# Kernel optimization log

Hardware: AMD Instinct MI355X
Metric: run time of the kernel (lower is better)

## Reference

```python
import jax, jax.numpy as jnp
import numpy as np

B, S, T = 8, 512, 512
E, NHEAD, HD = 512, 8, 64
SRC_VOCAB, TGT_VOCAB, WINDOW = 32000, 8000, 512
LN_EPS = 1e-3  # keras LayerNormalization default


def positional_encoding(length, depth):
    half = depth // 2
    positions = jnp.arange(length, dtype=jnp.float32)[:, None]
    depths = jnp.arange(half, dtype=jnp.float32)[None, :] / (depth / 2)
    angle_rates = 1.0 / (10000.0 ** depths)
    angle_rads = positions * angle_rates  # [length, half]
    return jnp.concatenate([jnp.sin(angle_rads), jnp.cos(angle_rads)], axis=-1)


def layer_norm(x, g, b):
    m = jnp.mean(x, axis=-1, keepdims=True)
    v = jnp.var(x, axis=-1, keepdims=True)
    return (x - m) * jax.lax.rsqrt(v + LN_EPS) * g + b


def mha(xk, xv, xq, wk, wv, wq, dw, db, causal):
    # wk/wv/wq: [H, E, HD] (stacked per-head weights, same math as naive per-head tensordots)
    K = jnp.einsum('bse,hed->bhsd', xk, wk)
    V = jnp.einsum('bse,hed->bhsd', xv, wv)
    Q = jnp.einsum('bqe,hed->bhqd', xq, wq)
    Sk = K.shape[2]
    # NOTE: original divides by sqrt(KEY SEQ LEN), not sqrt(head_dim)
    logits = jnp.einsum('bhqd,bhkd->bhqk', Q, K) / jnp.sqrt(jnp.float32(Sk))
    if causal:
        Sq = Q.shape[2]
        mask = jnp.triu(jnp.full((Sq, Sk), -jnp.inf, dtype=logits.dtype), k=1)
        logits = logits + mask
    w = jax.nn.softmax(logits, axis=-1)
    att = jnp.einsum('bhqk,bhkd->bhqd', w, V)
    b_, h_, q_, d_ = att.shape
    att = att.transpose(0, 2, 1, 3).reshape(b_, q_, h_ * d_)  # concat heads
    return att @ dw + db


def setup_inputs() -> dict:
    key = jax.random.key(0)
    ks = jax.random.split(key, 32)
    n = lambda i, shape, std=0.01: jax.random.normal(ks[i], shape, dtype=jnp.float32) * std
    inp = {
        'src_ids': jax.random.randint(ks[0], (B, S), 0, SRC_VOCAB, dtype=jnp.int32),
        'tgt_ids': jax.random.randint(ks[1], (B, T), 0, TGT_VOCAB, dtype=jnp.int32),
        'src_emb': n(2, (SRC_VOCAB, E), 0.05),
        'tgt_emb': n(3, (TGT_VOCAB, E), 0.05),
        # encoder block
        'enc_wk': n(4, (NHEAD, E, HD)), 'enc_wv': n(5, (NHEAD, E, HD)), 'enc_wq': n(6, (NHEAD, E, HD)),
        'enc_dw': n(7, (E, E), 0.02), 'enc_db': jnp.zeros((E,), jnp.float32),
        'enc_ffw': n(8, (E, E), 0.02), 'enc_ffb': jnp.zeros((E,), jnp.float32),
        'enc_ln_g': jnp.ones((E,), jnp.float32), 'enc_ln_b': jnp.zeros((E,), jnp.float32),
        # decoder block: self-attn, cross-attn, ff, shared ln
        'dec_swk': n(9, (NHEAD, E, HD)), 'dec_swv': n(10, (NHEAD, E, HD)), 'dec_swq': n(11, (NHEAD, E, HD)),
        'dec_sdw': n(12, (E, E), 0.02), 'dec_sdb': jnp.zeros((E,), jnp.float32),
        'dec_cwk': n(13, (NHEAD, E, HD)), 'dec_cwv': n(14, (NHEAD, E, HD)), 'dec_cwq': n(15, (NHEAD, E, HD)),
        'dec_cdw': n(16, (E, E), 0.02), 'dec_cdb': jnp.zeros((E,), jnp.float32),
        'dec_ffw': n(17, (E, E), 0.02), 'dec_ffb': jnp.zeros((E,), jnp.float32),
        'dec_ln_g': jnp.ones((E,), jnp.float32), 'dec_ln_b': jnp.zeros((E,), jnp.float32),
        # classifier
        'cls_w1': n(18, (E, 2 * TGT_VOCAB), 0.02), 'cls_b1': jnp.zeros((2 * TGT_VOCAB,), jnp.float32),
        'cls_w2': n(19, (2 * TGT_VOCAB, TGT_VOCAB), 0.02), 'cls_b2': jnp.zeros((TGT_VOCAB,), jnp.float32),
    }
    return inp


def reference(src_ids, tgt_ids, src_emb, tgt_emb,
              enc_wk, enc_wv, enc_wq, enc_dw, enc_db, enc_ffw, enc_ffb, enc_ln_g, enc_ln_b,
              dec_swk, dec_swv, dec_swq, dec_sdw, dec_sdb,
              dec_cwk, dec_cwv, dec_cwq, dec_cdw, dec_cdb,
              dec_ffw, dec_ffb, dec_ln_g, dec_ln_b,
              cls_w1, cls_b1, cls_w2, cls_b2):
    pos = positional_encoding(WINDOW, E)
    scale = jnp.sqrt(jnp.float32(E))
    x = src_emb[src_ids] * scale + pos[:src_ids.shape[1]]
    y = tgt_emb[tgt_ids] * scale + pos[:tgt_ids.shape[1]]

    # encoder block (self-attn is CAUSALLY masked in original: use_mask=True hardcoded)
    a = mha(x, x, x, enc_wk, enc_wv, enc_wq, enc_dw, enc_db, causal=True)
    h = layer_norm(x + a, enc_ln_g, enc_ln_b)
    f = h @ enc_ffw + enc_ffb
    enc_out = layer_norm(h + f, enc_ln_g, enc_ln_b)

    # decoder block
    sa = mha(y, y, y, dec_swk, dec_swv, dec_swq, dec_sdw, dec_sdb, causal=True)
    h1 = layer_norm(sa + y, dec_ln_g, dec_ln_b)
    ca = mha(enc_out, enc_out, h1, dec_cwk, dec_cwv, dec_cwq, dec_cdw, dec_cdb, causal=False)
    h2 = layer_norm(ca + h1, dec_ln_g, dec_ln_b)
    f2 = h2 @ dec_ffw + dec_ffb
    dec_out = jax.nn.relu(layer_norm(f2 + h2, dec_ln_g, dec_ln_b))

    # classifier
    hid = jax.nn.relu(dec_out @ cls_w1 + cls_b1)
    return hid @ cls_w2 + cls_b2
```

## Files before the change

kernel.cpp:

```cpp
#include <hip/hip_runtime.h>

#define SEQ 512
#define EDIM 512
#define NHEAD 8
#define HDIM 64
#define NBATCH 8
#define ROWS (NBATCH * SEQ)
#define QKV_N (3 * EDIM)
#define TGTV 8000
#define HID2 16000
#define LN_EPS 1e-3f

#define BM 128
#define BN 128
#define BK 32

typedef unsigned short u16;
typedef __bf16 bf16x8 __attribute__((ext_vector_type(8)));
typedef float f32x4 __attribute__((ext_vector_type(4)));

__device__ __forceinline__ float b2f(u16 x) {
  unsigned int u = ((unsigned int)x) << 16;
  float f;
  __builtin_memcpy(&f, &u, 4);
  return f;
}
__device__ __forceinline__ u16 f2b(float f) {
  unsigned int u;
  __builtin_memcpy(&u, &f, 4);
  u = (u + 0x7fffu + ((u >> 16) & 1u)) >> 16;
  return (u16)u;
}

__device__ __forceinline__ void async_copy16(const void* g, void* l) {
  __builtin_amdgcn_global_load_lds(
      (const __attribute__((address_space(1))) unsigned int*)g,
      (__attribute__((address_space(3))) unsigned int*)l, 16, 0, 0);
}

__global__ __launch_bounds__(256) void gemm_bt(
    const u16* __restrict__ A, const u16* __restrict__ B, void* __restrict__ C,
    const float* __restrict__ bias, int M, int N, int K, int lda, int ldb,
    int ldc, long abb, long abh, long bbb, long bbh, long cbb, long cbh,
    int nbh, int flags) {
  __shared__ __align__(16) u16 lsA[BM * BK];
  __shared__ __align__(16) u16 lsB[BN * BK];
  const int tid = threadIdx.x;
  const int wave = tid >> 6, lane = tid & 63;
  const int quad = lane >> 4, l16 = lane & 15;
  const int wm = (wave & 1) << 6, wn = (wave >> 1) << 6;

  const int z = blockIdx.z;
  const int zb = z / nbh, zh = z - zb * nbh;
  const u16* Ab = A + zb * abb + zh * abh;
  const u16* Bb = B + zb * bbb + zh * bbh;
  const long coff = zb * cbb + zh * cbh;
  const int m0 = blockIdx.y * BM, n0 = blockIdx.x * BN;

  f32x4 acc[4][4];
#pragma unroll
  for (int i = 0; i < 4; ++i)
#pragma unroll
    for (int j = 0; j < 4; ++j) acc[i][j] = (f32x4)0.0f;

  const int srow = tid >> 2;
  const int skc = (tid & 3) << 3;
  const u16* ga0 = Ab + (long)(m0 + srow) * lda + skc;
  const u16* ga1 = ga0 + 64L * lda;
  const u16* gb0 = Bb + (long)(n0 + srow) * ldb + skc;
  const u16* gb1 = gb0 + 64L * ldb;
  u16* la0 = &lsA[(wave << 6) * 8];
  u16* la1 = &lsA[(256 + (wave << 6)) * 8];
  u16* lb0 = &lsB[(wave << 6) * 8];
  u16* lb1 = &lsB[(256 + (wave << 6)) * 8];

  for (int k0 = 0; k0 < K; k0 += BK) {
    async_copy16(ga0 + k0, la0);
    async_copy16(ga1 + k0, la1);
    async_copy16(gb0 + k0, lb0);
    async_copy16(gb1 + k0, lb1);
    __syncthreads();
    bf16x8 af[4], bfr[4];
#pragma unroll
    for (int i = 0; i < 4; ++i)
      af[i] = *(const bf16x8*)&lsA[(wm + (i << 4) + l16) * BK + (quad << 3)];
#pragma unroll
    for (int j = 0; j < 4; ++j)
      bfr[j] = *(const bf16x8*)&lsB[(wn + (j << 4) + l16) * BK + (quad << 3)];
#pragma unroll
    for (int i = 0; i < 4; ++i)
#pragma unroll
      for (int j = 0; j < 4; ++j)
        acc[i][j] = __builtin_amdgcn_mfma_f32_16x16x32_bf16(af[i], bfr[j],
                                                            acc[i][j], 0, 0, 0);
    __syncthreads();
  }

  const int relu = flags & 1, obf = flags & 2;
  float bv[4];
#pragma unroll
  for (int j = 0; j < 4; ++j) {
    int col = n0 + wn + (j << 4) + l16;
    bv[j] = (bias != nullptr && col < N) ? bias[col] : 0.0f;
  }
#pragma unroll
  for (int i = 0; i < 4; ++i) {
    int rbase = m0 + wm + (i << 4) + (quad << 2);
#pragma unroll
    for (int j = 0; j < 4; ++j) {
      int col = n0 + wn + (j << 4) + l16;
      if (col < N) {
#pragma unroll
        for (int r = 0; r < 4; ++r) {
          float v = acc[i][j][r] + bv[j];
          if (relu) v = fmaxf(v, 0.0f);
          long idx = coff + (long)(rbase + r) * ldc + col;
          if (obf)
            ((u16*)C)[idx] = f2b(v);
          else
            ((float*)C)[idx] = v;
        }
      }
    }
  }
}

__device__ __forceinline__ float cvt_f(float x) { return x; }
__device__ __forceinline__ float cvt_f(u16 x) { return b2f(x); }

template <typename T>
__global__ __launch_bounds__(256) void transpose_k(
    const T* __restrict__ in, u16* __restrict__ out, int K, int N, int in_ld,
    int out_ld, long ib0, long ib1, long ob0, long ob1, int nb1) {
  __shared__ float tile[32][33];
  const int z = blockIdx.z;
  const int b0 = z / nb1, b1 = z - b0 * nb1;
  const T* ip = in + b0 * ib0 + b1 * ib1;
  u16* op = out + b0 * ob0 + b1 * ob1;
  const int tx = threadIdx.x & 31, ty = threadIdx.x >> 5;
  const int n = blockIdx.x * 32 + tx;
  const int kb = blockIdx.y * 32;
#pragma unroll
  for (int i = ty; i < 32; i += 8) {
    int k = kb + i;
    if (k < K && n < N) tile[i][tx] = cvt_f(ip[(long)k * in_ld + n]);
  }
  __syncthreads();
  const int k2 = kb + tx;
#pragma unroll
  for (int i = ty; i < 32; i += 8) {
    int n2 = blockIdx.x * 32 + i;
    if (k2 < K && n2 < N) op[(long)n2 * out_ld + k2] = f2b(tile[tx][i]);
  }
}

__device__ __forceinline__ float wave_red_max(float v) {
#pragma unroll
  for (int o = 32; o > 0; o >>= 1) v = fmaxf(v, __shfl_xor(v, o, 64));
  return v;
}
__device__ __forceinline__ float wave_red_sum(float v) {
#pragma unroll
  for (int o = 32; o > 0; o >>= 1) v += __shfl_xor(v, o, 64);
  return v;
}

__global__ __launch_bounds__(256) void softmax_k(const float* __restrict__ Sc,
                                                 u16* __restrict__ P,
                                                 int causal) {
  __shared__ float red[4];
  const int row = blockIdx.x;
  const int q = row & (SEQ - 1);
  const float* s = Sc + (long)row * SEQ;
  u16* p = P + (long)row * SEQ;
  const int lim = causal ? q : (SEQ - 1);
  const int t = threadIdx.x;
  const int wave = t >> 6, lane = t & 63;
  const float scale = 0.044194173824159216f;
  float v0 = (t <= lim) ? s[t] * scale : -3.0e38f;
  float v1 = (t + 256 <= lim) ? s[t + 256] * scale : -3.0e38f;
  float mxw = wave_red_max(fmaxf(v0, v1));
  if (lane == 0) red[wave] = mxw;
  __syncthreads();
  float mx = fmaxf(fmaxf(red[0], red[1]), fmaxf(red[2], red[3]));
  __syncthreads();
  float e0 = (t <= lim) ? expf(v0 - mx) : 0.0f;
  float e1 = (t + 256 <= lim) ? expf(v1 - mx) : 0.0f;
  float smw = wave_red_sum(e0 + e1);
  if (lane == 0) red[wave] = smw;
  __syncthreads();
  float inv = 1.0f / (red[0] + red[1] + red[2] + red[3]);
  p[t] = f2b(e0 * inv);
  p[t + 256] = f2b(e1 * inv);
}

__global__ __launch_bounds__(256) void add_ln_k(
    const u16* __restrict__ Xa, const u16* __restrict__ Xb,
    const float* __restrict__ g, const float* __restrict__ be,
    u16* __restrict__ O, int relu) {
  __shared__ float red[8];
  const int row = blockIdx.x;
  const int t = threadIdx.x;
  const int wave = t >> 6, lane = t & 63;
  const long base = (long)row * EDIM;
  float x0 = b2f(Xa[base + t]) + b2f(Xb[base + t]);
  float x1 = b2f(Xa[base + t + 256]) + b2f(Xb[base + t + 256]);
  float s = wave_red_sum(x0 + x1);
  float s2 = wave_red_sum(x0 * x0 + x1 * x1);
  if (lane == 0) {
    red[wave] = s;
    red[wave + 4] = s2;
  }
  __syncthreads();
  s = red[0] + red[1] + red[2] + red[3];
  s2 = red[4] + red[5] + red[6] + red[7];
  float mean = s * (1.0f / EDIM);
  float var = s2 * (1.0f / EDIM) - mean * mean;
  float r = rsqrtf(var + LN_EPS);
  float y0 = (x0 - mean) * r * g[t] + be[t];
  float y1 = (x1 - mean) * r * g[t + 256] + be[t + 256];
  if (relu) {
    y0 = fmaxf(y0, 0.0f);
    y1 = fmaxf(y1, 0.0f);
  }
  O[base + t] = f2b(y0);
  O[base + t + 256] = f2b(y1);
}

__global__ __launch_bounds__(256) void embed_k(const int* __restrict__ ids,
                                               const float* __restrict__ emb,
                                               u16* __restrict__ out) {
  const int row = blockIdx.x;
  const int t = threadIdx.x;
  const int s = row & (SEQ - 1);
  const int id = ids[row];
  const float* e = emb + (long)id * EDIM;
  const long base = (long)row * EDIM;
#pragma unroll
  for (int i = 0; i < 2; ++i) {
    int c = t + i * 256;
    int j = (c < 256) ? c : c - 256;
    float ang = (float)s * expf(-9.210340371976184f * ((float)j * (1.0f / 256.0f)));
    float pos = (c < 256) ? sinf(ang) : cosf(ang);
    out[base + c] = f2b(e[c] * 22.627416997969522f + pos);
  }
}

extern "C" void kernel_launch(void* const* d_in, const int* in_sizes, int n_in,
                              void* d_out, int out_size, void* d_ws,
                              size_t ws_size, hipStream_t stream) {
  const int* src_ids = (const int*)d_in[0];
  const int* tgt_ids = (const int*)d_in[1];
  const float* src_emb = (const float*)d_in[2];
  const float* tgt_emb = (const float*)d_in[3];
  const float* enc_wk = (const float*)d_in[4];
  const float* enc_wv = (const float*)d_in[5];
  const float* enc_wq = (const float*)d_in[6];
  const float* enc_dw = (const float*)d_in[7];
  const float* enc_db = (const float*)d_in[8];
  const float* enc_ffw = (const float*)d_in[9];
  const float* enc_ffb = (const float*)d_in[10];
  const float* enc_ln_g = (const float*)d_in[11];
  const float* enc_ln_b = (const float*)d_in[12];
  const float* dec_swk = (const float*)d_in[13];
  const float* dec_swv = (const float*)d_in[14];
  const float* dec_swq = (const float*)d_in[15];
  const float* dec_sdw = (const float*)d_in[16];
  const float* dec_sdb = (const float*)d_in[17];
  const float* dec_cwk = (const float*)d_in[18];
  const float* dec_cwv = (const float*)d_in[19];
  const float* dec_cwq = (const float*)d_in[20];
  const float* dec_cdw = (const float*)d_in[21];
  const float* dec_cdb = (const float*)d_in[22];
  const float* dec_ffw = (const float*)d_in[23];
  const float* dec_ffb = (const float*)d_in[24];
  const float* dec_ln_g = (const float*)d_in[25];
  const float* dec_ln_b = (const float*)d_in[26];
  const float* cls_w1 = (const float*)d_in[27];
  const float* cls_b1 = (const float*)d_in[28];
  const float* cls_w2 = (const float*)d_in[29];
  const float* cls_b2 = (const float*)d_in[30];
  (void)in_sizes; (void)n_in; (void)out_size; (void)ws_size;

  char* wsp = (char*)d_ws;
  size_t off = 0;
  auto alloc = [&](size_t bytes) -> char* {
    char* p = wsp + off;
    off += (bytes + 255) & ~(size_t)255;
    return p;
  };
  u16* x_bf = (u16*)alloc((size_t)ROWS * EDIM * 2);
  u16* y_bf = (u16*)alloc((size_t)ROWS * EDIM * 2);
  u16* wqkv_e = (u16*)alloc((size_t)QKV_N * EDIM * 2);
  u16* wqkv_s = (u16*)alloc((size_t)QKV_N * EDIM * 2);
  u16* wqkv_c = (u16*)alloc((size_t)QKV_N * EDIM * 2);
  u16* t_encdw = (u16*)alloc((size_t)EDIM * EDIM * 2);
  u16* t_encff = (u16*)alloc((size_t)EDIM * EDIM * 2);
  u16* t_sdw = (u16*)alloc((size_t)EDIM * EDIM * 2);
  u16* t_cdw = (u16*)alloc((size_t)EDIM * EDIM * 2);
  u16* t_decff = (u16*)alloc((size_t)EDIM * EDIM * 2);
  u16* w1t = (u16*)alloc((size_t)HID2 * EDIM * 2);
  u16* w2t = (u16*)alloc((size_t)8064 * HID2 * 2);
  u16* qkv = (u16*)alloc((size_t)ROWS * QKV_N * 2);
  float* scores = (float*)alloc((size_t)64 * SEQ * SEQ * 4);
  u16* pbf = (u16*)alloc((size_t)64 * SEQ * SEQ * 2);
  u16* vt = (u16*)alloc((size_t)64 * 128 * SEQ * 2);
  u16* att = (u16*)alloc((size_t)ROWS * EDIM * 2);
  u16* tmp = (u16*)alloc((size_t)ROWS * EDIM * 2);
  u16* hbf = (u16*)alloc((size_t)ROWS * EDIM * 2);
  u16* enc_o = (u16*)alloc((size_t)ROWS * EDIM * 2);
  u16* h1 = (u16*)alloc((size_t)ROWS * EDIM * 2);
  u16* h2 = (u16*)alloc((size_t)ROWS * EDIM * 2);
  u16* dec_o = (u16*)alloc((size_t)ROWS * EDIM * 2);
  u16* hid = (u16*)alloc((size_t)ROWS * HID2 * 2);

  auto gemm = [&](const u16* A, const u16* Bt, void* C, const float* bias,
                  int M, int N, int K, int lda, int ldb, int ldc, long abb,
                  long abh, long bbb, long bbh, long cbb, long cbh, int nbh,
                  int nz, int flags) {
    dim3 grid((N + BN - 1) / BN, (M + BM - 1) / BM, nz);
    gemm_bt<<<grid, dim3(256), 0, stream>>>(A, Bt, C, bias, M, N, K, lda, ldb,
                                            ldc, abb, abh, bbb, bbh, cbb, cbh,
                                            nbh, flags);
  };
  auto trf = [&](const float* in, u16* out, int K, int N, int ild, int old_,
                 long ib0, long ib1, long ob0, long ob1, int nb0, int nb1) {
    dim3 grid((N + 31) / 32, (K + 31) / 32, nb0 * nb1);
    transpose_k<float><<<grid, dim3(256), 0, stream>>>(in, out, K, N, ild,
                                                       old_, ib0, ib1, ob0,
                                                       ob1, nb1);
  };
  auto trb = [&](const u16* in, u16* out, int K, int N, int ild, int old_,
                 long ib0, long ib1, long ob0, long ob1, int nb0, int nb1) {
    dim3 grid((N + 31) / 32, (K + 31) / 32, nb0 * nb1);
    transpose_k<u16><<<grid, dim3(256), 0, stream>>>(in, out, K, N, ild, old_,
                                                     ib0, ib1, ob0, ob1, nb1);
  };

  embed_k<<<dim3(ROWS), dim3(256), 0, stream>>>(src_ids, src_emb, x_bf);
  embed_k<<<dim3(ROWS), dim3(256), 0, stream>>>(tgt_ids, tgt_emb, y_bf);

  auto repack_qkv = [&](const float* wq, const float* wk, const float* wv,
                        u16* dst) {
    trf(wq, dst, EDIM, HDIM, HDIM, EDIM, 0, (long)EDIM * HDIM, 0,
        (long)HDIM * EDIM, 1, NHEAD);
    trf(wk, dst + EDIM * EDIM, EDIM, HDIM, HDIM, EDIM, 0, (long)EDIM * HDIM, 0,
        (long)HDIM * EDIM, 1, NHEAD);
    trf(wv, dst + 2 * EDIM * EDIM, EDIM, HDIM, HDIM, EDIM, 0,
        (long)EDIM * HDIM, 0, (long)HDIM * EDIM, 1, NHEAD);
  };
  repack_qkv(enc_wq, enc_wk, enc_wv, wqkv_e);
  repack_qkv(dec_swq, dec_swk, dec_swv, wqkv_s);
  repack_qkv(dec_cwq, dec_cwk, dec_cwv, wqkv_c);
  trf(enc_dw, t_encdw, EDIM, EDIM, EDIM, EDIM, 0, 0, 0, 0, 1, 1);
  trf(enc_ffw, t_encff, EDIM, EDIM, EDIM, EDIM, 0, 0, 0, 0, 1, 1);
  trf(dec_sdw, t_sdw, EDIM, EDIM, EDIM, EDIM, 0, 0, 0, 0, 1, 1);
  trf(dec_cdw, t_cdw, EDIM, EDIM, EDIM, EDIM, 0, 0, 0, 0, 1, 1);
  trf(dec_ffw, t_decff, EDIM, EDIM, EDIM, EDIM, 0, 0, 0, 0, 1, 1);
  trf(cls_w1, w1t, EDIM, HID2, HID2, EDIM, 0, 0, 0, 0, 1, 1);
  trf(cls_w2, w2t, HID2, TGTV, TGTV, HID2, 0, 0, 0, 0, 1, 1);

  const long SB = (long)SEQ * QKV_N;
  const long SS = (long)SEQ * SEQ;
  const long VTB = 128L * SEQ;

  auto attention = [&](int causal) {
    trb(qkv + 2 * EDIM, vt, SEQ, HDIM, QKV_N, SEQ, SB, HDIM, 8 * VTB, VTB,
        NBATCH, NHEAD);
    gemm(qkv, qkv + EDIM, scores, nullptr, SEQ, SEQ, HDIM, QKV_N, QKV_N, SEQ,
         SB, HDIM, SB, HDIM, 8 * SS, SS, NHEAD, 64, 0);
    softmax_k<<<dim3(64 * SEQ), dim3(256), 0, stream>>>(scores, pbf, causal);
    gemm(pbf, vt, att, nullptr, SEQ, HDIM, SEQ, SEQ, SEQ, EDIM, 8 * SS, SS,
         8 * VTB, VTB, (long)SEQ * EDIM, HDIM, NHEAD, 64, 2);
  };

  gemm(x_bf, wqkv_e, qkv, nullptr, ROWS, QKV_N, EDIM, EDIM, EDIM, QKV_N, 0, 0,
       0, 0, 0, 0, 1, 1, 2);
  attention(1);
  gemm(att, t_encdw, tmp, enc_db, ROWS, EDIM, EDIM, EDIM, EDIM, EDIM, 0, 0, 0,
       0, 0, 0, 1, 1, 2);
  add_ln_k<<<dim3(ROWS), dim3(256), 0, stream>>>(x_bf, tmp, enc_ln_g, enc_ln_b,
                                                 hbf, 0);
  gemm(hbf, t_encff, tmp, enc_ffb, ROWS, EDIM, EDIM, EDIM, EDIM, EDIM, 0, 0, 0,
       0, 0, 0, 1, 1, 2);
  add_ln_k<<<dim3(ROWS), dim3(256), 0, stream>>>(hbf, tmp, enc_ln_g, enc_ln_b,
                                                 enc_o, 0);

  gemm(y_bf, wqkv_s, qkv, nullptr, ROWS, QKV_N, EDIM, EDIM, EDIM, QKV_N, 0, 0,
       0, 0, 0, 0, 1, 1, 2);
  attention(1);
  gemm(att, t_sdw, tmp, dec_sdb, ROWS, EDIM, EDIM, EDIM, EDIM, EDIM, 0, 0, 0,
       0, 0, 0, 1, 1, 2);
  add_ln_k<<<dim3(ROWS), dim3(256), 0, stream>>>(y_bf, tmp, dec_ln_g, dec_ln_b,
                                                 h1, 0);

  gemm(h1, wqkv_c, qkv, nullptr, ROWS, EDIM, EDIM, EDIM, EDIM, QKV_N, 0, 0, 0,
       0, 0, 0, 1, 1, 2);
  gemm(enc_o, wqkv_c + EDIM * EDIM, qkv + EDIM, nullptr, ROWS, 2 * EDIM, EDIM,
       EDIM, EDIM, QKV_N, 0, 0, 0, 0, 0, 0, 1, 1, 2);
  attention(0);
  gemm(att, t_cdw, tmp, dec_cdb, ROWS, EDIM, EDIM, EDIM, EDIM, EDIM, 0, 0, 0,
       0, 0, 0, 1, 1, 2);
  add_ln_k<<<dim3(ROWS), dim3(256), 0, stream>>>(h1, tmp, dec_ln_g, dec_ln_b,
                                                 h2, 0);

  gemm(h2, t_decff, tmp, dec_ffb, ROWS, EDIM, EDIM, EDIM, EDIM, EDIM, 0, 0, 0,
       0, 0, 0, 1, 1, 2);
  add_ln_k<<<dim3(ROWS), dim3(256), 0, stream>>>(h2, tmp, dec_ln_g, dec_ln_b,
                                                 dec_o, 1);

  gemm(dec_o, w1t, hid, cls_b1, ROWS, HID2, EDIM, EDIM, EDIM, HID2, 0, 0, 0, 0,
       0, 0, 1, 1, 3);
  gemm(hid, w2t, d_out, cls_b2, ROWS, TGTV, HID2, HID2, HID2, TGTV, 0, 0, 0, 0,
       0, 0, 1, 1, 0);
}
```

Baseline: 3.332 ms.

## Add 256x256 double-buffered async-copy GEMM kernel for classifier layers

```diff
diff --git a/kernel.cpp b/kernel.cpp
--- a/kernel.cpp
+++ b/kernel.cpp
@@ -115,6 +115,173 @@
           float v = acc[i][j][r] + bv[j];
           if (relu) v = fmaxf(v, 0.0f);
           long idx = coff + (long)(rbase + r) * ldc + col;
+          if (obf)
+            ((u16*)C)[idx] = f2b(v);
+          else
+            ((float*)C)[idx] = v;
+        }
+      }
+    }
+  }
+}
+
+__global__ __launch_bounds__(512, 2) void gemm_big(
+    const u16* __restrict__ A, const u16* __restrict__ B, void* __restrict__ C,
+    const float* __restrict__ bias, int M, int N, int K, int lda, int ldb,
+    int ldc, int nblast, int flags) {
+  __shared__ __align__(16) u16 lds[2][2][2][8192];
+  const int tid = threadIdx.x;
+  const int wave = tid >> 6, lane = tid & 63;
+  const int quad = lane >> 4, l16 = lane & 15;
+  const int wmi = wave >> 2, wni = wave & 3;
+  (void)M;
+
+  const int gx = gridDim.x, gy = gridDim.y;
+  const int nwg = gx * gy;
+  const int orig = blockIdx.y * gx + blockIdx.x;
+  const int q8 = nwg >> 3, r8 = nwg & 7;
+  const int xcd = orig & 7, i8 = orig >> 3;
+  const int wg =
+      (xcd < r8 ? xcd * (q8 + 1) : r8 * (q8 + 1) + (xcd - r8) * q8) + i8;
+  const int m0 = (wg % gy) * 256;
+  const int n0 = (wg / gy) * 256;
+
+  const int stid = tid ^ (((tid >> 5) & 1) << 1);
+  const int srow = stid >> 3;
+  const int scol = (stid & 7) << 3;
+  const u16* gA00 = A + (long)(m0 + srow) * lda + scol;
+  const u16* gA01 = A + (long)(m0 + 64 + srow) * lda + scol;
+  const u16* gA10 = A + (long)(m0 + 128 + srow) * lda + scol;
+  const u16* gA11 = A + (long)(m0 + 192 + srow) * lda + scol;
+  const int rb0 = min(n0 + srow, nblast);
+  const int rb1 = min(n0 + 64 + srow, nblast);
+  const int rb2 = min(n0 + 128 + srow, nblast);
+  const int rb3 = min(n0 + 192 + srow, nblast);
+  const u16* gB00 = B + (long)rb0 * ldb + scol;
+  const u16* gB01 = B + (long)rb1 * ldb + scol;
+  const u16* gB10 = B + (long)rb2 * ldb + scol;
+  const u16* gB11 = B + (long)rb3 * ldb + scol;
+  u16* lp = &lds[0][0][0][0];
+  const int wo = wave << 9;
+
+#define STAGE(DD, KOFF)                              \
+  do {                                               \
+    u16* lb_ = lp + (DD) * 32768 + wo;               \
+    async_copy16(gA00 + (KOFF), lb_ + 0);            \
+    async_copy16(gA01 + (KOFF), lb_ + 4096);         \
+    async_copy16(gA10 + (KOFF), lb_ + 8192);         \
+    async_copy16(gA11 + (KOFF), lb_ + 12288);        \
+    async_copy16(gB00 + (KOFF), lb_ + 16384);        \
+    async_copy16(gB01 + (KOFF), lb_ + 20480);        \
+    async_copy16(gB10 + (KOFF), lb_ + 24576);        \
+    async_copy16(gB11 + (KOFF), lb_ + 28672);        \
+  } while (0)
+
+  const int rxor = ((l16 >> 2) & 1) << 5;
+  const int kq0 = (quad << 4) ^ rxor;
+  const int kq1 = (64 | (quad << 4)) ^ rxor;
+  const char* ldsc = (const char*)lp;
+
+  f32x4 acc[8][4];
+#pragma unroll
+  for (int i = 0; i < 8; ++i)
+#pragma unroll
+    for (int j = 0; j < 4; ++j) acc[i][j] = (f32x4)0.0f;
+  bf16x8 af[4][2];
+  bf16x8 bfr[2][2];
+
+#define LDA_Q(QM)                                                             \
+  do {                                                                        \
+    const char* pa_ =                                                         \
+        ldsc + dOff + (wmi << 14) + ((QM) << 13) + (l16 << 7);                \
+    _Pragma("unroll") for (int mf4 = 0; mf4 < 4; ++mf4) {                     \
+      af[mf4][0] = *(const bf16x8*)(pa_ + mf4 * 2048 + kq0);                  \
+      af[mf4][1] = *(const bf16x8*)(pa_ + mf4 * 2048 + kq1);                  \
+    }                                                                         \
+  } while (0)
+
+#define LDB_Q(QN)                                                             \
+  do {                                                                        \
+    const char* pb_ = ldsc + dOff + 32768 + ((wni >> 1) << 14) +              \
+                      ((wni & 1) << 13) + ((QN) << 12) + (l16 << 7);          \
+    _Pragma("unroll") for (int nf2 = 0; nf2 < 2; ++nf2) {                     \
+      bfr[nf2][0] = *(const bf16x8*)(pb_ + nf2 * 2048 + kq0);                 \
+      bfr[nf2][1] = *(const bf16x8*)(pb_ + nf2 * 2048 + kq1);                 \
+    }                                                                         \
+  } while (0)
+
+#define MMA_Q(QM, QN)                                                         \
+  do {                                                                        \
+    __builtin_amdgcn_s_setprio(1);                                            \
+    _Pragma("unroll") for (int ks = 0; ks < 2; ++ks)                          \
+        _Pragma("unroll") for (int mf4 = 0; mf4 < 4; ++mf4)                   \
+            _Pragma("unroll") for (int nf2 = 0; nf2 < 2; ++nf2)               \
+                acc[(QM) * 4 + mf4][(QN) * 2 + nf2] =                         \
+        __builtin_amdgcn_mfma_f32_16x16x32_bf16(                              \
+            af[mf4][ks], bfr[nf2][ks], acc[(QM) * 4 + mf4][(QN) * 2 + nf2],   \
+            0, 0, 0);                                                         \
+    __builtin_amdgcn_s_setprio(0);                                            \
+  } while (0)
+
+#define BAR()                          \
+  do {                                 \
+    asm volatile("" ::: "memory");     \
+    __builtin_amdgcn_s_barrier();      \
+    asm volatile("" ::: "memory");     \
+  } while (0)
+
+  const int NT = K >> 6;
+  STAGE(0, 0L);
+  STAGE(1, 64L);
+
+  for (int t = 0; t < NT; ++t) {
+    const int dOff = (t & 1) * 65536;
+    if (t + 1 < NT)
+      asm volatile("s_waitcnt vmcnt(8)" ::: "memory");
+    else
+      asm volatile("s_waitcnt vmcnt(0)" ::: "memory");
+    BAR();
+    LDA_Q(0);
+    LDB_Q(0);
+    MMA_Q(0, 0);
+    BAR();
+    LDB_Q(1);
+    MMA_Q(0, 1);
+    BAR();
+    LDA_Q(1);
+    MMA_Q(1, 1);
+    BAR();
+    LDB_Q(0);
+    MMA_Q(1, 0);
+    BAR();
+    if (t + 2 < NT) STAGE(t & 1, (long)(t + 2) << 6);
+  }
+
+#undef STAGE
+#undef LDA_Q
+#undef LDB_Q
+#undef MMA_Q
+#undef BAR
+
+  const int relu = flags & 1, obf = flags & 2;
+  float bv[4];
+#pragma unroll
+  for (int nf = 0; nf < 4; ++nf) {
+    int col = n0 + (wni << 6) + (nf << 4) + l16;
+    bv[nf] = (bias != nullptr && col < N) ? bias[col] : 0.0f;
+  }
+#pragma unroll
+  for (int mf = 0; mf < 8; ++mf) {
+    int rbase = m0 + (wmi << 7) + (mf << 4) + (quad << 2);
+#pragma unroll
+    for (int nf = 0; nf < 4; ++nf) {
+      int col = n0 + (wni << 6) + (nf << 4) + l16;
+      if (col < N) {
+#pragma unroll
+        for (int r = 0; r < 4; ++r) {
+          float v = acc[mf][nf][r] + bv[nf];
+          if (relu) v = fmaxf(v, 0.0f);
+          long idx = (long)(rbase + r) * ldc + col;
           if (obf)
             ((u16*)C)[idx] = f2b(v);
           else
@@ -323,6 +490,13 @@
                                             ldc, abb, abh, bbb, bbh, cbb, cbh,
                                             nbh, flags);
   };
+  auto gemm_big_l = [&](const u16* A, const u16* Bt, void* C,
+                        const float* bias, int M, int N, int K, int lda,
+                        int ldb, int ldc, int nblast, int flags) {
+    dim3 grid((N + 255) / 256, M / 256, 1);
+    gemm_big<<<grid, dim3(512), 0, stream>>>(A, Bt, C, bias, M, N, K, lda,
+                                             ldb, ldc, nblast, flags);
+  };
   auto trf = [&](const float* in, u16* out, int K, int N, int ild, int old_,
                  long ib0, long ib1, long ob0, long ob1, int nb0, int nb1) {
     dim3 grid((N + 31) / 32, (K + 31) / 32, nb0 * nb1);
@@ -409,8 +583,8 @@
   add_ln_k<<<dim3(ROWS), dim3(256), 0, stream>>>(h2, tmp, dec_ln_g, dec_ln_b,
                                                  dec_o, 1);
 
-  gemm(dec_o, w1t, hid, cls_b1, ROWS, HID2, EDIM, EDIM, EDIM, HID2, 0, 0, 0, 0,
-       0, 0, 1, 1, 3);
-  gemm(hid, w2t, d_out, cls_b2, ROWS, TGTV, HID2, HID2, HID2, TGTV, 0, 0, 0, 0,
-       0, 0, 1, 1, 0);
-}
+  gemm_big_l(dec_o, w1t, hid, cls_b1, ROWS, HID2, EDIM, EDIM, EDIM, HID2,
+             HID2 - 1, 3);
+  gemm_big_l(hid, w2t, d_out, cls_b2, ROWS, TGTV, HID2, HID2, HID2, TGTV,
+             8063, 0);
+}
```

Result: faster. 2.670 ms (-19.9%).
